# Kernel tuning notes

Measured on AMD Instinct MI355X. Metric: run time of the kernel, lower is better.

Reference implementation:

```python
import jax, jax.numpy as jnp
import numpy as np

B, T, D = 2, 2048, 2048
N_HEADS, N_KV, HEAD_DIM = 8, 4, 256
S_CACHE = 2048
WINDOW = 512
SOFT_CAP = 50.0
ROPE_TS = 10000
ROPE_PROP = 1.0
EPS = 1e-6
NEG_INF = -2.3819763e38


def setup_inputs() -> dict:
    key = jax.random.key(0)
    ks = jax.random.split(key, 6)
    x = jax.random.normal(ks[0], (B, T, D), dtype=jnp.float32)
    wq = jax.random.normal(ks[1], (D, N_HEADS * HEAD_DIM), dtype=jnp.float32) * (D ** -0.5)
    wk = jax.random.normal(ks[2], (D, N_KV * HEAD_DIM), dtype=jnp.float32) * (D ** -0.5)
    wv = jax.random.normal(ks[3], (D, N_KV * HEAD_DIM), dtype=jnp.float32) * (D ** -0.5)
    wo = jax.random.normal(ks[4], (N_HEADS * HEAD_DIM, D), dtype=jnp.float32) * ((N_HEADS * HEAD_DIM) ** -0.5)
    return {
        'x': x,
        'segment_pos': jnp.broadcast_to(jnp.arange(T, dtype=jnp.int32), (B, T)),
        'cur_ind': 0,
        'wq': wq, 'wk': wk, 'wv': wv, 'wo': wo,
        'q_norm_scale': jnp.zeros((HEAD_DIM,), jnp.float32),
        'k_norm_scale': jnp.zeros((HEAD_DIM,), jnp.float32),
        'k_cache': jnp.zeros((B, S_CACHE, N_KV, HEAD_DIM), jnp.float32),
        'v_cache': jnp.zeros((B, S_CACHE, N_KV, HEAD_DIM), jnp.float32),
    }


def _rms_norm(x, scale, eps=EPS):
    # Gemma4RMSNorm: fp32 norm, (1 + scale) offset
    xf = x.astype(jnp.float32)
    n = xf * jax.lax.rsqrt(jnp.mean(jnp.square(xf), -1, keepdims=True) + eps)
    return (n * (1.0 + scale)).astype(x.dtype)


def _apply_rope(x, pos, max_timescale=ROPE_TS, proportion=ROPE_PROP):
    # x: [B, T, n, H]; pos: [B, T]. Partial RoPE on first proportion*H dims.
    H = x.shape[-1]
    rope_dim = int(H * proportion)
    half = rope_dim // 2
    frac = jnp.arange(half, dtype=jnp.float32) / half
    timescale = jnp.asarray(max_timescale, jnp.float32) ** frac  # [half]
    sinusoid = pos.astype(jnp.float32)[..., None] / timescale    # [B, T, half]
    sin = jnp.sin(sinusoid)[:, :, None, :]
    cos = jnp.cos(sinusoid)[:, :, None, :]
    x_rope, x_pass = x[..., :rope_dim], x[..., rope_dim:]
    x1, x2 = x_rope[..., :half], x_rope[..., half:]
    rotated = jnp.concatenate([x1 * cos - x2 * sin, x2 * cos + x1 * sin], axis=-1)
    return jnp.concatenate([rotated, x_pass], axis=-1).astype(x.dtype)


def reference(x, segment_pos, cur_ind, wq, wk, wv, wo, q_norm_scale, k_norm_scale, k_cache, v_cache):
    b, t, _ = x.shape
    g = N_HEADS // N_KV  # GQA group size

    q = (x @ wq).reshape(b, t, N_HEADS, HEAD_DIM)
    k = (x @ wk).reshape(b, t, N_KV, HEAD_DIM)
    v = (x @ wv).reshape(b, t, N_KV, HEAD_DIM)

    # QK-norm (per-head RMSNorm) then RoPE
    q = _rms_norm(q, q_norm_scale)
    k = _rms_norm(k, k_norm_scale)
    q = _apply_rope(q, segment_pos)
    k = _apply_rope(k, segment_pos)

    # KV-cache scatter write at cur_ind
    idx = jnp.asarray(cur_ind, jnp.int32)
    k_cache = jax.lax.dynamic_update_slice(k_cache, k, (0, idx, 0, 0))
    v_cache = jax.lax.dynamic_update_slice(v_cache, v, (0, idx, 0, 0))

    # Attention logits over full cache: [b, kv, g, t, s]
    qg = q.reshape(b, t, N_KV, g, HEAD_DIM) * (HEAD_DIM ** -0.5)
    logits = jnp.einsum('btkgh,bskh->bkgts', qg, k_cache)
    logits = SOFT_CAP * jnp.tanh(logits / SOFT_CAP)

    # Causal + sliding-window mask from absolute positions
    q_pos = segment_pos[:, :, None]                              # [b, t, 1]
    k_pos = jnp.arange(S_CACHE, dtype=jnp.int32)[None, None, :]  # [1, 1, s]
    mask = (k_pos <= q_pos) & (q_pos - k_pos < WINDOW)           # [b, t, s]
    logits = jnp.where(mask[:, None, None, :, :], logits, NEG_INF)

    probs = jax.nn.softmax(logits, axis=-1)
    attn = jnp.einsum('bkgts,bskh->btkgh', probs, v_cache).reshape(b, t, N_HEADS * HEAD_DIM)
    return attn @ wo
```

## Files before the change

### kernel.cpp

```cpp
#include <hip/hip_runtime.h>

#define T_SEQ 2048
#define NHEADS 8
#define NKV 4
#define HD 256
#define WIN 512

typedef __bf16 bf16x8 __attribute__((ext_vector_type(8)));
typedef float f32x4 __attribute__((ext_vector_type(4)));

__device__ __forceinline__ float bf2f(unsigned short u) {
    return __uint_as_float(((unsigned int)u) << 16);
}
__device__ __forceinline__ unsigned short f2bf(float f) {
    unsigned int u = __float_as_uint(f);
    u += 0x7fffu + ((u >> 16) & 1u);
    return (unsigned short)(u >> 16);
}

#define GLOAD_LDS16(gptr, lptr)                                            \
    __builtin_amdgcn_global_load_lds(                                      \
        (const __attribute__((address_space(1))) unsigned int*)(gptr),     \
        (__attribute__((address_space(3))) unsigned int*)(lptr), 16, 0, 0)

__global__ void detect_dtype(const unsigned short* __restrict__ x, int* flag) {
    int tid = threadIdx.x;
    int cnt = 0;
    for (int i = 0; i < 64; ++i) {
        unsigned short u = x[2 * (tid * 64 + i)];
        int e = (u >> 7) & 0xFF;
        cnt += (e >= 100 && e <= 140) ? 1 : 0;
    }
    #pragma unroll
    for (int o = 32; o >= 1; o >>= 1) cnt += __shfl_xor(cnt, o);
    if (tid == 0) *flag = (cnt > 2048) ? 1 : 0;
}

__device__ __forceinline__ void dev_convert8(
    const void* src, unsigned short* dst, int isb, int i)
{
    if (isb) {
        *(uint4*)&dst[i] = *(const uint4*)((const unsigned short*)src + i);
    } else {
        const float* s = (const float*)src + i;
        unsigned short v[8];
        #pragma unroll
        for (int j = 0; j < 8; ++j) v[j] = f2bf(s[j]);
        *(uint4*)&dst[i] = *(uint4*)v;
    }
}

__device__ __forceinline__ void dev_transpose32(
    const void* src, unsigned short* dst, int isb, int R, int C,
    int bx, int by, int tid, unsigned short (*tile)[33])
{
    const int c = tid & 31, r8 = tid >> 5;
    #pragma unroll
    for (int i = 0; i < 4; ++i) {
        int r = r8 + i * 8;
        size_t idx = (size_t)(by * 32 + r) * C + bx * 32 + c;
        tile[r][c] = isb ? ((const unsigned short*)src)[idx]
                         : f2bf(((const float*)src)[idx]);
    }
    __syncthreads();
    #pragma unroll
    for (int i = 0; i < 4; ++i) {
        int r = r8 + i * 8;
        dst[(size_t)(bx * 32 + r) * R + by * 32 + c] = tile[c][r];
    }
}

__device__ __forceinline__ void dev_finalize(
    unsigned short* qkv, const int* segment_pos,
    const void* qs_raw, const void* ks_raw, int isb, int w, int lane)
{
    const int b = w / (T_SEQ * 12);
    const int rem = w % (T_SEQ * 12);
    const int t = rem / 12;
    const int slot = rem % 12;
    const bool isq = slot < 8;
    const int col0 = isq ? slot * 256 : 2048 + (slot - 8) * 256;
    unsigned short* p = qkv + (size_t)(b * T_SEQ + t) * 4096 + col0;

    float e[4];
    #pragma unroll
    for (int j = 0; j < 4; ++j) e[j] = bf2f(p[lane + 64 * j]);
    float ss = e[0] * e[0] + e[1] * e[1] + e[2] * e[2] + e[3] * e[3];
    #pragma unroll
    for (int o = 32; o >= 1; o >>= 1) ss += __shfl_xor(ss, o);
    const float rn = rsqrtf(ss * (1.0f / 256.0f) + 1e-6f);
    const void* scp = isq ? qs_raw : ks_raw;
    float nrm[4];
    #pragma unroll
    for (int j = 0; j < 4; ++j) {
        float sc = isb ? bf2f(((const unsigned short*)scp)[lane + 64 * j])
                       : ((const float*)scp)[lane + 64 * j];
        nrm[j] = e[j] * rn * (1.0f + sc);
    }

    const int pos = segment_pos[b * T_SEQ + t];
    #pragma unroll
    for (int pp = 0; pp < 2; ++pp) {
        const int i = lane + 64 * pp;
        const float inv_ts = __expf((float)i * -0.07195578415606293f);
        float s, c;
        __sincosf((float)pos * inv_ts, &s, &c);
        const float x1 = nrm[pp], x2 = nrm[pp + 2];
        p[i]       = f2bf(x1 * c - x2 * s);
        p[i + 128] = f2bf(x2 * c + x1 * s);
    }
}

__device__ __forceinline__ void dev_build_vt(
    const unsigned short* qkv, unsigned short* vt,
    int bx, int by, int bz, int tid, unsigned short (*tile)[33])
{
    const int bkv = bz;
    const int b = bkv >> 2, kv = bkv & 3;
    const int s0 = bx * 32, d0 = by * 32;
    const int c = tid & 31, r8 = tid >> 5;
    #pragma unroll
    for (int i = 0; i < 4; ++i) {
        int r = r8 + i * 8;
        tile[r][c] = qkv[(size_t)(b * T_SEQ + s0 + r) * 4096 + 3072 + kv * 256 + d0 + c];
    }
    __syncthreads();
    #pragma unroll
    for (int i = 0; i < 4; ++i) {
        int r = r8 + i * 8;
        vt[((size_t)bkv * 256 + d0 + r) * T_SEQ + s0 + c] = tile[c][r];
    }
}

__global__ __launch_bounds__(256) void convert_to_bf16(
    const void* __restrict__ src, unsigned short* __restrict__ dst,
    const int* __restrict__ flag, int n)
{
    int i = (blockIdx.x * 256 + threadIdx.x) * 8;
    if (i >= n) return;
    dev_convert8(src, dst, *flag, i);
}

__global__ __launch_bounds__(256) void transpose_cvt(
    const void* __restrict__ src, unsigned short* __restrict__ dst,
    const int* __restrict__ flag, int R, int C)
{
    __shared__ unsigned short tile[32][33];
    dev_transpose32(src, dst, *flag, R, C, blockIdx.x, blockIdx.y,
                    threadIdx.x, tile);
}

__global__ __launch_bounds__(256) void finalize_qk(
    unsigned short* __restrict__ qkv,
    const int* __restrict__ segment_pos,
    const void* __restrict__ qs_raw,
    const void* __restrict__ ks_raw,
    const int* __restrict__ flag)
{
    dev_finalize(qkv, segment_pos, qs_raw, ks_raw, *flag,
                 blockIdx.x * 4 + (threadIdx.x >> 6), threadIdx.x & 63);
}

__global__ __launch_bounds__(256) void build_vt(
    const unsigned short* __restrict__ qkv, unsigned short* __restrict__ vt)
{
    __shared__ unsigned short tile[32][33];
    dev_build_vt(qkv, vt, blockIdx.x, blockIdx.y, blockIdx.z,
                 threadIdx.x, tile);
}

__global__ __launch_bounds__(256) void prep_fused(
    const void* __restrict__ x,
    const void* __restrict__ wq, const void* __restrict__ wk,
    const void* __restrict__ wv,
    unsigned short* __restrict__ xhat, unsigned short* __restrict__ wT,
    const int* __restrict__ flag)
{
    __shared__ unsigned short tile[32][33];
    const int bid = blockIdx.x;
    const int tid = threadIdx.x;
    const int isb = *flag;
    if (bid < 4096) {
        dev_convert8(x, xhat, isb, (bid * 256 + tid) * 8);
    } else {
        const int k = bid - 4096;
        const int bx = k % 128, by = k / 128;
        const void* src; int C, rowoff, cb;
        if (bx < 64)      { src = wq; C = 2048; rowoff = 0;    cb = bx; }
        else if (bx < 96) { src = wk; C = 1024; rowoff = 2048; cb = bx - 64; }
        else              { src = wv; C = 1024; rowoff = 3072; cb = bx - 96; }
        dev_transpose32(src, wT + (size_t)rowoff * 2048, isb, 2048, C,
                        cb, by, tid, tile);
    }
}

__global__ __launch_bounds__(256) void post_fused(
    unsigned short* __restrict__ qkv,
    const int* __restrict__ segment_pos,
    const void* __restrict__ qs_raw, const void* __restrict__ ks_raw,
    unsigned short* __restrict__ vt,
    const void* __restrict__ wo, unsigned short* __restrict__ woT,
    const int* __restrict__ flag)
{
    __shared__ unsigned short tile[32][33];
    const int bid = blockIdx.x;
    const int tid = threadIdx.x;
    if (bid < 12288) {
        dev_finalize(qkv, segment_pos, qs_raw, ks_raw, *flag,
                     bid * 4 + (tid >> 6), tid & 63);
    } else if (bid < 16384) {
        const int k = bid - 12288;
        dev_build_vt(qkv, vt, k % 64, (k / 64) % 8, k / 512, tid, tile);
    } else {
        const int k = bid - 16384;
        dev_transpose32(wo, woT, *flag, 2048, 2048, k % 64, k / 64, tid, tile);
    }
}

__global__ __launch_bounds__(256) void gemm_bf16(
    const unsigned short* __restrict__ A,
    const unsigned short* __restrict__ Bt,
    void* __restrict__ C,
    int M, int Ntot, int K, int n_base,
    const int* __restrict__ flag, int force_bf16)
{
    __shared__ __align__(16) unsigned short As[128 * 32];
    __shared__ __align__(16) unsigned short Bs[128 * 32];
    const int tid = threadIdx.x;
    const int n0 = blockIdx.x * 128;
    const int m0 = blockIdx.y * 128;
    const int wave = tid >> 6;
    const int lane = tid & 63;
    const int wm = (wave >> 1) * 64;
    const int wn = (wave & 1) * 64;
    const int quad = lane >> 4;
    const int l16 = lane & 15;
    const int obf = force_bf16 | *flag;

    f32x4 acc[4][4];
    #pragma unroll
    for (int i = 0; i < 4; ++i)
        #pragma unroll
        for (int j = 0; j < 4; ++j)
            acc[i][j] = f32x4{0.f, 0.f, 0.f, 0.f};

    for (int kk = 0; kk < K; kk += 32) {
        #pragma unroll
        for (int i = 0; i < 2; ++i) {
            int ch = tid + i * 256;
            int row = ch >> 2;
            int ko = (ch & 3) * 8;
            GLOAD_LDS16(&A[(size_t)(m0 + row) * K + kk + ko],  &As[ch * 8]);
            GLOAD_LDS16(&Bt[(size_t)(n0 + row) * K + kk + ko], &Bs[ch * 8]);
        }
        __syncthreads();
        bf16x8 af[4], bfr[4];
        #pragma unroll
        for (int mi = 0; mi < 4; ++mi)
            af[mi] = *(const bf16x8*)&As[(wm + mi * 16 + l16) * 32 + quad * 8];
        #pragma unroll
        for (int ni = 0; ni < 4; ++ni)
            bfr[ni] = *(const bf16x8*)&Bs[(wn + ni * 16 + l16) * 32 + quad * 8];
        #pragma unroll
        for (int mi = 0; mi < 4; ++mi)
            #pragma unroll
            for (int ni = 0; ni < 4; ++ni)
                acc[mi][ni] = __builtin_amdgcn_mfma_f32_16x16x32_bf16(
                    af[mi], bfr[ni], acc[mi][ni], 0, 0, 0);
        __syncthreads();
    }

    #pragma unroll
    for (int mi = 0; mi < 4; ++mi)
        #pragma unroll
        for (int ni = 0; ni < 4; ++ni)
            #pragma unroll
            for (int r = 0; r < 4; ++r) {
                int row = m0 + wm + mi * 16 + quad * 4 + r;
                int col = n_base + n0 + wn + ni * 16 + l16;
                size_t idx = (size_t)row * Ntot + col;
                if (obf) ((unsigned short*)C)[idx] = f2bf(acc[mi][ni][r]);
                else     ((float*)C)[idx]          = acc[mi][ni][r];
            }
}

__global__ __launch_bounds__(512, 2) void gemm256_bf16(
    const unsigned short* __restrict__ A,
    const unsigned short* __restrict__ Bt,
    void* __restrict__ C,
    int M, int Ntot, int K, int n_base, int gx,
    const int* __restrict__ flag, int force_bf16)
{
    __shared__ __align__(16) unsigned short A_lds[2][256 * 64];
    __shared__ __align__(16) unsigned short B_lds[2][256 * 64];

    const int tid = threadIdx.x;
    const int cpx = gridDim.x >> 3;
    const int swzb = (blockIdx.x & 7) * cpx + (blockIdx.x >> 3);
    const int bx = swzb % gx, by = swzb / gx;
    const int n0 = bx * 256, m0 = by * 256;

    const int wave = tid >> 6, lane = tid & 63;
    const int wr = wave >> 2, wc = wave & 3;
    const int quad = lane >> 4, l16 = lane & 15;
    const int sw7 = l16 & 7;
    const int obf = force_bf16 | *flag;

    const int trow = tid >> 3;
    const int tg   = tid & 7;
    const int tsw  = (tg ^ (trow & 7)) * 8;

    f32x4 acc[8][4];
    #pragma unroll
    for (int i = 0; i < 8; ++i)
        #pragma unroll
        for (int j = 0; j < 4; ++j)
            acc[i][j] = f32x4{0.f, 0.f, 0.f, 0.f};

    const int NT = K >> 6;
    const int NI = NT >> 1;

#define STAGE_A(d_, hm_, kt_)                                                  \
    do { _Pragma("unroll") for (int j = 0; j < 2; ++j) {                       \
        int r_ = j * 128 + (hm_) * 64 + trow;                                  \
        GLOAD_LDS16(&A[(size_t)(m0 + r_) * K + (kt_) * 64 + tsw],              \
                    &A_lds[d_][((hm_) * 128 + j * 64 + trow) * 64 + tg * 8]);  \
    } } while (0)

#define STAGE_B(d_, hn_, kt_)                                                  \
    do { _Pragma("unroll") for (int j = 0; j < 2; ++j) {                       \
        int w2_ = j * 64 + trow;                                               \
        int r_ = (w2_ >> 5) * 64 + (hn_) * 32 + (w2_ & 31);                    \
        GLOAD_LDS16(&Bt[(size_t)(n0 + r_) * K + (kt_) * 64 + tsw],             \
                    &B_lds[d_][((hn_) * 128 + w2_) * 64 + tg * 8]);            \
    } } while (0)

    bf16x8 a[4][2], b0[2][2], b1[2][2];

#define LDA_H(d_, hm_)                                                         \
    do { _Pragma("unroll") for (int mi = 0; mi < 4; ++mi)                      \
         _Pragma("unroll") for (int ks = 0; ks < 2; ++ks)                      \
            a[mi][ks] = *(const bf16x8*)&A_lds[d_][                            \
                ((hm_) * 128 + wr * 64 + mi * 16 + l16) * 64                   \
                + (((ks * 4 + quad) ^ sw7) * 8)]; } while (0)

#define LDB_H(d_, hn_, bb_)                                                    \
    do { _Pragma("unroll") for (int ni = 0; ni < 2; ++ni)                      \
         _Pragma("unroll") for (int ks = 0; ks < 2; ++ks)                      \
            bb_[ni][ks] = *(const bf16x8*)&B_lds[d_][                          \
                ((hn_) * 128 + wc * 32 + ni * 16 + l16) * 64                   \
                + (((ks * 4 + quad) ^ sw7) * 8)]; } while (0)

#define MFMAQ(hm_, hn_, bb_)                                                   \
    do { __builtin_amdgcn_s_setprio(1);                                        \
         _Pragma("unroll") for (int mi = 0; mi < 4; ++mi)                      \
         _Pragma("unroll") for (int ni = 0; ni < 2; ++ni)                      \
         _Pragma("unroll") for (int ks = 0; ks < 2; ++ks)                      \
            acc[(hm_) * 4 + mi][(hn_) * 2 + ni] =                              \
                __builtin_amdgcn_mfma_f32_16x16x32_bf16(                       \
                    a[mi][ks], bb_[ni][ks],                                    \
                    acc[(hm_) * 4 + mi][(hn_) * 2 + ni], 0, 0, 0);             \
         __builtin_amdgcn_s_setprio(0); } while (0)

#define BAR() do { __builtin_amdgcn_sched_barrier(0);                          \
                   __builtin_amdgcn_s_barrier();                               \
                   __builtin_amdgcn_sched_barrier(0); } while (0)
#define LGKM0() do { asm volatile("s_waitcnt lgkmcnt(0)" ::: "memory");        \
                     __builtin_amdgcn_sched_barrier(0); } while (0)
#define VMC(n_) asm volatile("s_waitcnt vmcnt(" #n_ ")" ::: "memory")

    STAGE_A(0, 0, 0); STAGE_B(0, 0, 0); STAGE_B(0, 1, 0); STAGE_A(0, 1, 0);
    STAGE_A(1, 0, 1); STAGE_B(1, 0, 1); STAGE_B(1, 1, 1);
    VMC(6);
    BAR();

    for (int i = 0; i < NI; ++i) {
        const int t2 = 2 * i + 2, t3 = 2 * i + 3;
        const bool s2 = t2 < NT, s3 = t3 < NT;

        LDA_H(0, 0); LDB_H(0, 0, b0);
        STAGE_A(1, 1, 2 * i + 1);
        BAR(); LGKM0(); MFMAQ(0, 0, b0);
        BAR();
        LDB_H(0, 1, b1);
        if (s2) STAGE_A(0, 0, t2);
        BAR(); LGKM0(); MFMAQ(0, 1, b1);
        BAR();
        LDA_H(0, 1);
        if (s2) STAGE_B(0, 0, t2);
        BAR(); LGKM0(); MFMAQ(1, 1, b1);
        BAR();
        if (s2) STAGE_B(0, 1, t2);
        BAR(); LGKM0(); MFMAQ(1, 0, b0);
        if (s2) { VMC(6); } else { VMC(0); }
        BAR();
        LDA_H(1, 0); LDB_H(1, 0, b0);
        if (s2) STAGE_A(0, 1, t2);
        BAR(); LGKM0(); MFMAQ(0, 0, b0);
        BAR();
        LDB_H(1, 1, b1);
        if (s3) STAGE_A(1, 0, t3);
        BAR(); LGKM0(); MFMAQ(0, 1, b1);
        BAR();
        LDA_H(1, 1);
        if (s3) STAGE_B(1, 0, t3);
        BAR(); LGKM0(); MFMAQ(1, 1, b1);
        BAR();
        if (s3) STAGE_B(1, 1, t3);
        BAR(); LGKM0(); MFMAQ(1, 0, b0);
        if (s3) { VMC(6); } else { VMC(0); }
        BAR();
    }

#undef STAGE_A
#undef STAGE_B
#undef LDA_H
#undef LDB_H
#undef MFMAQ
#undef BAR
#undef LGKM0
#undef VMC

    #pragma unroll
    for (int mi = 0; mi < 8; ++mi)
        #pragma unroll
        for (int ni = 0; ni < 4; ++ni)
            #pragma unroll
            for (int r = 0; r < 4; ++r) {
                int row = m0 + wr * 128 + mi * 16 + quad * 4 + r;
                int col = n_base + n0 + wc * 64 + ni * 16 + l16;
                size_t idx = (size_t)row * Ntot + col;
                if (obf) ((unsigned short*)C)[idx] = f2bf(acc[mi][ni][r]);
                else     ((float*)C)[idx]          = acc[mi][ni][r];
            }
}

__global__ __launch_bounds__(512, 2) void gemm128n_bf16(
    const unsigned short* __restrict__ A,
    const unsigned short* __restrict__ Bt,
    void* __restrict__ C,
    int M, int Ntot, int K, int n_base, int gx,
    const int* __restrict__ flag, int force_bf16)
{
    __shared__ __align__(16) unsigned short A_lds[2][256 * 64];
    __shared__ __align__(16) unsigned short B_lds[2][128 * 64];

    const int tid = threadIdx.x;
    const int cpx = gridDim.x >> 3;
    const int swzb = (blockIdx.x & 7) * cpx + (blockIdx.x >> 3);
    const int bx = swzb % gx, by = swzb / gx;
    const int n0 = bx * 128, m0 = by * 256;

    const int wave = tid >> 6, lane = tid & 63;
    const int wr = wave >> 2, wc = wave & 3;
    const int quad = lane >> 4, l16 = lane & 15;
    const int sw7 = l16 & 7;
    const int obf = force_bf16 | *flag;

    const int r0 = tid >> 3;
    const int chs = ((tid & 7) ^ (r0 & 7)) * 8;
    const unsigned short* Ab = A  + (size_t)(m0 + r0) * K + chs;
    const unsigned short* Bb = Bt + (size_t)(n0 + r0) * K + chs;

    f32x4 acc[8][2];
    #pragma unroll
    for (int i = 0; i < 8; ++i)
        #pragma unroll
        for (int j = 0; j < 2; ++j)
            acc[i][j] = f32x4{0.f, 0.f, 0.f, 0.f};

    const int NT = K >> 6;

#define STAGE_N(buf_, kt_)                                                \
    do {                                                                  \
        _Pragma("unroll")                                                 \
        for (int j = 0; j < 4; ++j)                                       \
            GLOAD_LDS16(Ab + (size_t)(64 * j) * K + (size_t)(kt_) * 64,   \
                        &A_lds[buf_][(tid + 512 * j) * 8]);               \
        _Pragma("unroll")                                                 \
        for (int j = 0; j < 2; ++j)                                       \
            GLOAD_LDS16(Bb + (size_t)(64 * j) * K + (size_t)(kt_) * 64,   \
                        &B_lds[buf_][(tid + 512 * j) * 8]);               \
    } while (0)

    STAGE_N(0, 0);
    __syncthreads();

    for (int t = 0; t < NT; ++t) {
        const int cb = t & 1;
        if (t + 1 < NT) STAGE_N(cb ^ 1, t + 1);

        const unsigned short* Ac = A_lds[cb];
        const unsigned short* Bc = B_lds[cb];
        bf16x8 a4[4][2], b2[2][2];

        #pragma unroll
        for (int ni = 0; ni < 2; ++ni)
            #pragma unroll
            for (int ks = 0; ks < 2; ++ks)
                b2[ni][ks] = *(const bf16x8*)&Bc[(wc * 32 + ni * 16 + l16) * 64
                                                + (((ks * 4 + quad) ^ sw7) * 8)];

        #pragma unroll
        for (int mi = 0; mi < 4; ++mi)
            #pragma unroll
            for (int ks = 0; ks < 2; ++ks)
                a4[mi][ks] = *(const bf16x8*)&Ac[(wr * 128 + mi * 16 + l16) * 64
                                                + (((ks * 4 + quad) ^ sw7) * 8)];
        __builtin_amdgcn_s_setprio(1);
        #pragma unroll
        for (int mi = 0; mi < 4; ++mi)
            #pragma unroll
            for (int ni = 0; ni < 2; ++ni)
                #pragma unroll
                for (int ks = 0; ks < 2; ++ks)
                    acc[mi][ni] = __builtin_amdgcn_mfma_f32_16x16x32_bf16(
                        a4[mi][ks], b2[ni][ks], acc[mi][ni], 0, 0, 0);
        __builtin_amdgcn_s_setprio(0);

        #pragma unroll
        for (int mi = 0; mi < 4; ++mi)
            #pragma unroll
            for (int ks = 0; ks < 2; ++ks)
                a4[mi][ks] = *(const bf16x8*)&Ac[(wr * 128 + (mi + 4) * 16 + l16) * 64
                                                + (((ks * 4 + quad) ^ sw7) * 8)];
        __builtin_amdgcn_s_setprio(1);
        #pragma unroll
        for (int mi = 0; mi < 4; ++mi)
            #pragma unroll
            for (int ni = 0; ni < 2; ++ni)
                #pragma unroll
                for (int ks = 0; ks < 2; ++ks)
                    acc[mi + 4][ni] = __builtin_amdgcn_mfma_f32_16x16x32_bf16(
                        a4[mi][ks], b2[ni][ks], acc[mi + 4][ni], 0, 0, 0);
        __builtin_amdgcn_s_setprio(0);

        __syncthreads();
    }
#undef STAGE_N

    #pragma unroll
    for (int mi = 0; mi < 8; ++mi)
        #pragma unroll
        for (int ni = 0; ni < 2; ++ni)
            #pragma unroll
            for (int r = 0; r < 4; ++r) {
                int row = m0 + wr * 128 + mi * 16 + quad * 4 + r;
                int col = n_base + n0 + wc * 32 + ni * 16 + l16;
                size_t idx = (size_t)row * Ntot + col;
                if (obf) ((unsigned short*)C)[idx] = f2bf(acc[mi][ni][r]);
                else     ((float*)C)[idx]          = acc[mi][ni][r];
            }
}

#define PSTR 80
#define ABAR() do { __builtin_amdgcn_sched_barrier(0);                         \
                    __builtin_amdgcn_s_barrier();                              \
                    __builtin_amdgcn_sched_barrier(0); } while (0)
__global__ __launch_bounds__(512, 1) void attn_mfma(
    const unsigned short* __restrict__ qkv,
    const unsigned short* __restrict__ vt,
    unsigned short* __restrict__ out)
{
    __shared__ __align__(16) unsigned short SMEM[16384 + 16384 + 8 * 16 * PSTR];
    unsigned short* K_lds  = SMEM;
    unsigned short* VT_lds = SMEM + 16384;

    const int tid = threadIdx.x;
    const int wave = tid >> 6, lane = tid & 63;
    const int l16 = lane & 15, quad = lane >> 4;
    const int sw = l16 & 7;
    const int bkv = blockIdx.x & 7;
    const int qt  = blockIdx.x >> 3;
    const int b = bkv >> 2, kvh = bkv & 3;
    const int t0 = qt * 64;
    const int h = kvh * 2 + (wave & 1);
    const int rowg = wave >> 1;
    const int woff = rowg * 16;
    const int tq = t0 + woff + l16;
    unsigned short* P_lds = SMEM + 32768 + wave * 16 * PSTR;

    bf16x8 qf[8];
    {
        const unsigned short* qp =
            qkv + (size_t)(b * T_SEQ + tq) * 4096 + h * 256 + quad * 8;
        #pragma unroll
        for (int c = 0; c < 8; ++c) qf[c] = *(const bf16x8*)(qp + 32 * c);
    }

    f32x4 o[16];
    #pragma unroll
    for (int nt = 0; nt < 16; ++nt) o[nt] = f32x4{0.f, 0.f, 0.f, 0.f};
    float l_run = 0.f;

    int s_lo = t0 - (WIN - 1); if (s_lo < 0) s_lo = 0;
    const int s_base = s_lo & ~63;
    const int s_last = t0 + 63;
    const int tqmin = t0 + woff;
    const int tqmax = tqmin + 15;
    const int wlo   = tqmin - (WIN - 1);
    const size_t kgbase = (size_t)b * T_SEQ * 4096 + 2048 + kvh * 256;
    const size_t vgbase = (size_t)bkv * 256 * T_SEQ;

    for (int sb = s_base; sb <= s_last; sb += 64) {
        ABAR();

        #pragma unroll
        for (int i = 0; i < 4; ++i) {
            int ch = tid + 512 * i;
            int row = ch >> 5, e8 = ch & 31;
            GLOAD_LDS16(&qkv[kgbase + (size_t)(sb + row) * 4096
                             + ((e8 ^ (row & 7)) * 8)],
                        &K_lds[ch * 8]);
        }
        #pragma unroll
        for (int i = 0; i < 4; ++i) {
            int ch = tid + 512 * i;
            int dr = ch >> 3, e8 = ch & 7;
            GLOAD_LDS16(&vt[vgbase + (size_t)dr * T_SEQ + sb
                            + ((e8 ^ (dr & 7)) * 8)],
                        &VT_lds[ch * 8]);
        }
        asm volatile("s_waitcnt vmcnt(4)" ::: "memory");
        ABAR();

        const bool act = !(sb > tqmax || sb + 63 < wlo);

        f32x4 st[4];
        #pragma unroll
        for (int mt = 0; mt < 4; ++mt) st[mt] = f32x4{0.f, 0.f, 0.f, 0.f};
        if (act) {
            __builtin_amdgcn_s_setprio(1);
            #pragma unroll
            for (int c = 0; c < 8; ++c) {
                bf16x8 kf[4];
                #pragma unroll
                for (int mt = 0; mt < 4; ++mt)
                    kf[mt] = *(const bf16x8*)&K_lds[(mt * 16 + l16) * 256 + (((4 * c + quad) ^ sw) * 8)];
                #pragma unroll
                for (int mt = 0; mt < 4; ++mt)
                    st[mt] = __builtin_amdgcn_mfma_f32_16x16x32_bf16(kf[mt], qf[c], st[mt], 0, 0, 0);
            }
            __builtin_amdgcn_s_setprio(0);

            #pragma unroll
            for (int mt = 0; mt < 4; ++mt)
                #pragma unroll
                for (int r = 0; r < 4; ++r) {
                    int sp = sb + mt * 16 + quad * 4 + r;
                    float e2 = __expf(st[mt][r] * 0.0025f);
                    float p = __expf(20.0f - 100.0f / (e2 + 1.0f));
                    bool valid = (sp <= tq) && (tq - sp < WIN);
                    p = valid ? p : 0.0f;
                    l_run += p;
                    P_lds[l16 * PSTR + mt * 16 + quad * 4 + r] = f2bf(p);
                }
        }

        asm volatile("s_waitcnt vmcnt(0)" ::: "memory");
        ABAR();

        if (act) {
            #pragma unroll
            for (int c = 0; c < 2; ++c) {
                bf16x8 pf = *(const bf16x8*)&P_lds[l16 * PSTR + 32 * c + quad * 8];
                __builtin_amdgcn_s_setprio(1);
                #pragma unroll
                for (int nt = 0; nt < 16; ++nt) {
                    bf16x8 vf = *(const bf16x8*)&VT_lds[(nt * 16 + l16) * 64 + (((4 * c + quad) ^ sw) * 8)];
                    o[nt] = __builtin_amdgcn_mfma_f32_16x16x32_bf16(pf, vf, o[nt], 0, 0, 0);
                }
                __builtin_amdgcn_s_setprio(0);
            }
        }
    }

    l_run += __shfl_xor(l_run, 16);
    l_run += __shfl_xor(l_run, 32);
    float linv[4];
    #pragma unroll
    for (int r = 0; r < 4; ++r) linv[r] = 1.0f / __shfl(l_run, quad * 4 + r);

    __syncthreads();
    unsigned short* W = SMEM + wave * (16 * 264);
    #pragma unroll
    for (int nt = 0; nt < 16; ++nt)
        #pragma unroll
        for (int r = 0; r < 4; ++r)
            W[(quad * 4 + r) * 264 + nt * 16 + l16] = f2bf(o[nt][r] * linv[r]);
    const int lr = lane >> 2, lc = (lane & 3) * 64;
    unsigned short* ob = out + (size_t)(b * T_SEQ + t0 + woff + lr) * 2048 + h * 256 + lc;
    #pragma unroll
    for (int j = 0; j < 8; ++j)
        *(uint4*)(ob + j * 8) = *(const uint4*)&W[lr * 264 + lc + j * 8];
}

extern "C" void kernel_launch(void* const* d_in, const int* in_sizes, int n_in,
                              void* d_out, int out_size, void* d_ws, size_t ws_size,
                              hipStream_t stream) {
    const void* x   = d_in[0];
    const int*  sp  = (const int*)d_in[1];
    const void* wq  = d_in[3];
    const void* wk  = d_in[4];
    const void* wv  = d_in[5];
    const void* wo  = d_in[6];
    const void* qsc = d_in[7];
    const void* ksc = d_in[8];

    unsigned short* ws = (unsigned short*)d_ws;
    int*            flag = (int*)ws;
    unsigned short* qkv  = (unsigned short*)d_out;
    dim3 blk(256);

    const size_t NEED = (size_t)(2048 + 8388608 + 8388608) * sizeof(unsigned short);

    const long long NXE = 4096LL * 2048LL;
    if ((long long)in_sizes[0] == NXE * 4)
        hipMemsetAsync(flag, 0, 4, stream);
    else if ((long long)in_sizes[0] == NXE * 2)
        hipMemsetAsync(flag, 1, 4, stream);
    else
        detect_dtype<<<1, 64, 0, stream>>>((const unsigned short*)x, flag);

    if (ws_size >= NEED) {
        unsigned short* xhat = ws + 2048;
        unsigned short* wT   = xhat + (size_t)4096 * 2048;
        unsigned short* abuf = xhat;
        unsigned short* vtb  = wT;
        unsigned short* woT  = wT + (size_t)2048 * 2048;

        prep_fused<<<12288, blk, 0, stream>>>(x, wq, wk, wv, xhat, wT, flag);

        gemm256_bf16<<<256, 512, 0, stream>>>(xhat, wT, qkv,
                                              4096, 4096, 2048, 0, 16, flag, 1);

        post_fused<<<20480, blk, 0, stream>>>(qkv, sp, qsc, ksc, vtb, wo, woT, flag);

        attn_mfma<<<256, 512, 0, stream>>>(qkv, vtb, abuf);

        gemm128n_bf16<<<256, 512, 0, stream>>>(abuf, woT, d_out,
                                               4096, 2048, 2048, 0, 16, flag, 0);
    } else {
        unsigned short* reg1 = ws + 2048;
        unsigned short* reg2 = reg1 + (size_t)4096 * 2048;
        unsigned short* xhat = reg1;
        unsigned short* abuf = reg1;

        convert_to_bf16<<<4096, blk, 0, stream>>>(x, xhat, flag, 4096 * 2048);

        transpose_cvt<<<dim3(64, 64), blk, 0, stream>>>(wq, reg2, flag, 2048, 2048);
        gemm_bf16<<<dim3(16, 32), blk, 0, stream>>>(xhat, reg2, qkv,
                                                    4096, 4096, 2048, 0, flag, 1);
        transpose_cvt<<<dim3(32, 64), blk, 0, stream>>>(wk, reg2,                     flag, 2048, 1024);
        transpose_cvt<<<dim3(32, 64), blk, 0, stream>>>(wv, reg2 + (size_t)1024*2048, flag, 2048, 1024);
        gemm_bf16<<<dim3(16, 32), blk, 0, stream>>>(xhat, reg2, qkv,
                                                    4096, 4096, 2048, 2048, flag, 1);

        finalize_qk<<<12288, blk, 0, stream>>>(qkv, sp, qsc, ksc, flag);

        build_vt<<<dim3(64, 8, 8), blk, 0, stream>>>(qkv, reg2);
        attn_mfma<<<256, 512, 0, stream>>>(qkv, reg2, abuf);

        transpose_cvt<<<dim3(64, 64), blk, 0, stream>>>(wo, reg2, flag, 2048, 2048);
        gemm_bf16<<<dim3(16, 32), blk, 0, stream>>>(abuf, reg2, d_out,
                                                    4096, 2048, 2048, 0, flag, 0);
    }
}
```

Baseline: 341.4 us.

## Fuse QK RMS-norm and RoPE into the QKV GEMM epilogue

Moves the per-head RMSNorm and rotary embedding for Q and K out of the post-processing kernel and into the epilogue of the 256x256 QKV GEMM. Each 256-column tile is exactly one head, so row sums of squares are reduced across waves through LDS, and the normalized values are staged in LDS so that the rotate-half pairs can be combined before writing bf16. This removes a full read-modify-write pass over Q and K and shrinks the post_fused grid. In exchange the GEMM epilogue gets more barriers, LDS traffic, transcendental work and register pressure.

```diff
diff --git a/kernel.cpp b/kernel.cpp
--- a/kernel.cpp
+++ b/kernel.cpp
@@ -195,9 +195,7 @@
 }
 
 __global__ __launch_bounds__(256) void post_fused(
-    unsigned short* __restrict__ qkv,
-    const int* __restrict__ segment_pos,
-    const void* __restrict__ qs_raw, const void* __restrict__ ks_raw,
+    const unsigned short* __restrict__ qkv,
     unsigned short* __restrict__ vt,
     const void* __restrict__ wo, unsigned short* __restrict__ woT,
     const int* __restrict__ flag)
@@ -205,14 +203,10 @@
     __shared__ unsigned short tile[32][33];
     const int bid = blockIdx.x;
     const int tid = threadIdx.x;
-    if (bid < 12288) {
-        dev_finalize(qkv, segment_pos, qs_raw, ks_raw, *flag,
-                     bid * 4 + (tid >> 6), tid & 63);
-    } else if (bid < 16384) {
-        const int k = bid - 12288;
-        dev_build_vt(qkv, vt, k % 64, (k / 64) % 8, k / 512, tid, tile);
+    if (bid < 4096) {
+        dev_build_vt(qkv, vt, bid % 64, (bid / 64) % 8, bid / 512, tid, tile);
     } else {
-        const int k = bid - 16384;
+        const int k = bid - 4096;
         dev_transpose32(wo, woT, *flag, 2048, 2048, k % 64, k / 64, tid, tile);
     }
 }
@@ -284,27 +278,30 @@
             }
 }
 
-__global__ __launch_bounds__(512, 2) void gemm256_bf16(
+__global__ __launch_bounds__(512, 2) void gemm256_qkv(
     const unsigned short* __restrict__ A,
     const unsigned short* __restrict__ Bt,
-    void* __restrict__ C,
-    int M, int Ntot, int K, int n_base, int gx,
-    const int* __restrict__ flag, int force_bf16)
+    unsigned short* __restrict__ qkv,
+    const int* __restrict__ segment_pos,
+    const void* __restrict__ qs_raw,
+    const void* __restrict__ ks_raw,
+    const int* __restrict__ flag)
 {
     __shared__ __align__(16) unsigned short A_lds[2][256 * 64];
     __shared__ __align__(16) unsigned short B_lds[2][256 * 64];
 
+    const int K = 2048;
     const int tid = threadIdx.x;
     const int cpx = gridDim.x >> 3;
     const int swzb = (blockIdx.x & 7) * cpx + (blockIdx.x >> 3);
-    const int bx = swzb % gx, by = swzb / gx;
+    const int bx = swzb % 16, by = swzb / 16;
     const int n0 = bx * 256, m0 = by * 256;
 
     const int wave = tid >> 6, lane = tid & 63;
     const int wr = wave >> 2, wc = wave & 3;
     const int quad = lane >> 4, l16 = lane & 15;
     const int sw7 = l16 & 7;
-    const int obf = force_bf16 | *flag;
+    const int isb = *flag;
 
     const int trow = tid >> 3;
     const int tg   = tid & 7;
@@ -421,18 +418,91 @@
 #undef LGKM0
 #undef VMC
 
+    if (bx >= 12) {
+        #pragma unroll
+        for (int mi = 0; mi < 8; ++mi)
+            #pragma unroll
+            for (int ni = 0; ni < 4; ++ni)
+                #pragma unroll
+                for (int r = 0; r < 4; ++r) {
+                    int row = m0 + wr * 128 + mi * 16 + quad * 4 + r;
+                    int col = n0 + wc * 64 + ni * 16 + l16;
+                    qkv[(size_t)row * 4096 + col] = f2bf(acc[mi][ni][r]);
+                }
+        return;
+    }
+
+    float* red = (float*)A_lds;
+    float* ex  = (float*)((char*)A_lds + 4096);
+
     #pragma unroll
     for (int mi = 0; mi < 8; ++mi)
         #pragma unroll
+        for (int r = 0; r < 4; ++r) {
+            float p = 0.f;
+            #pragma unroll
+            for (int ni = 0; ni < 4; ++ni)
+                p += acc[mi][ni][r] * acc[mi][ni][r];
+            p += __shfl_xor(p, 1);
+            p += __shfl_xor(p, 2);
+            p += __shfl_xor(p, 4);
+            p += __shfl_xor(p, 8);
+            if (l16 == 0)
+                red[(wr * 4 + wc) * 128 + mi * 16 + quad * 4 + r] = p;
+        }
+    __syncthreads();
+    float rn_[8][4];
+    #pragma unroll
+    for (int mi = 0; mi < 8; ++mi)
+        #pragma unroll
+        for (int r = 0; r < 4; ++r) {
+            int rl = mi * 16 + quad * 4 + r;
+            float s = red[(wr * 4 + 0) * 128 + rl] + red[(wr * 4 + 1) * 128 + rl]
+                    + red[(wr * 4 + 2) * 128 + rl] + red[(wr * 4 + 3) * 128 + rl];
+            rn_[mi][r] = rsqrtf(s * (1.0f / 256.0f) + 1e-6f);
+        }
+
+    const void* scp = (bx < 8) ? qs_raw : ks_raw;
+    float sc[4];
+    #pragma unroll
+    for (int ni = 0; ni < 4; ++ni) {
+        int d = wc * 64 + ni * 16 + l16;
+        sc[ni] = 1.0f + (isb ? bf2f(((const unsigned short*)scp)[d])
+                             : ((const float*)scp)[d]);
+    }
+    float it_[4];
+    #pragma unroll
+    for (int ni = 0; ni < 4; ++ni)
+        it_[ni] = __expf((float)(wc * 64 + ni * 16 + l16) * -0.07195578415606293f);
+
+    for (int mi = 0; mi < 8; ++mi) {
+        __syncthreads();
+        #pragma unroll
         for (int ni = 0; ni < 4; ++ni)
             #pragma unroll
-            for (int r = 0; r < 4; ++r) {
-                int row = m0 + wr * 128 + mi * 16 + quad * 4 + r;
-                int col = n_base + n0 + wc * 64 + ni * 16 + l16;
-                size_t idx = (size_t)row * Ntot + col;
-                if (obf) ((unsigned short*)C)[idx] = f2bf(acc[mi][ni][r]);
-                else     ((float*)C)[idx]          = acc[mi][ni][r];
+            for (int r = 0; r < 4; ++r)
+                ex[(wr * 16 + quad * 4 + r) * 256 + wc * 64 + ni * 16 + l16] =
+                    acc[mi][ni][r] * rn_[mi][r] * sc[ni];
+        __syncthreads();
+        if (wc < 2) {
+            #pragma unroll
+            for (int ni = 0; ni < 4; ++ni) {
+                const int col = wc * 64 + ni * 16 + l16;
+                #pragma unroll
+                for (int r = 0; r < 4; ++r) {
+                    const int row = m0 + wr * 128 + mi * 16 + quad * 4 + r;
+                    const float x1 = ex[(wr * 16 + quad * 4 + r) * 256 + col];
+                    const float x2 = ex[(wr * 16 + quad * 4 + r) * 256 + col + 128];
+                    const int pos = segment_pos[row];
+                    float s_, c_;
+                    __sincosf((float)pos * it_[ni], &s_, &c_);
+                    unsigned short* q = qkv + (size_t)row * 4096 + n0;
+                    q[col]       = f2bf(x1 * c_ - x2 * s_);
+                    q[col + 128] = f2bf(x2 * c_ + x1 * s_);
+                }
             }
+        }
+    }
 }
 
 __global__ __launch_bounds__(512, 2) void gemm128n_bf16(
@@ -731,10 +801,9 @@
 
         prep_fused<<<12288, blk, 0, stream>>>(x, wq, wk, wv, xhat, wT, flag);
 
-        gemm256_bf16<<<256, 512, 0, stream>>>(xhat, wT, qkv,
-                                              4096, 4096, 2048, 0, 16, flag, 1);
-
-        post_fused<<<20480, blk, 0, stream>>>(qkv, sp, qsc, ksc, vtb, wo, woT, flag);
+        gemm256_qkv<<<256, 512, 0, stream>>>(xhat, wT, qkv, sp, qsc, ksc, flag);
+
+        post_fused<<<8192, blk, 0, stream>>>(qkv, vtb, wo, woT, flag);
 
         attn_mfma<<<256, 512, 0, stream>>>(qkv, vtb, abuf);
 
```

Result: slower. 395.5 us (+15.8%).
